# Kernel tuning notes

Measured on AMD Instinct MI355X. Metric: run time of the kernel, lower is better.

The kernel has to match this reference:

```python
import jax, jax.numpy as jnp
import numpy as np

B, N, D = 1024, 7, 1024
SQRT_D = float(np.sqrt(D))
MAX_CTX, MAX_VIB = 0.24, 0.26
VIB_IDX, CTX_IDX = 3, N - 1

ADJ = jnp.asarray(np.array([
    [1, 1, 0, 0, 1, 1, 1],
    [1, 1, 1, 1, 1, 1, 1],
    [0, 1, 1, 0, 1, 0, 1],
    [0, 1, 0, 1, 1, 1, 1],
    [1, 1, 1, 1, 1, 1, 1],
    [1, 1, 0, 1, 1, 1, 1],
    [1, 1, 1, 1, 1, 1, 1]], dtype=np.float32))


def _gelu(x):
    return jax.nn.gelu(x, approximate=False)


def setup_inputs() -> dict:
    key = jax.random.key(0)
    ks = jax.random.split(key, 20)
    s = 0.02
    def w(k, shape):
        return jax.random.normal(k, shape, dtype=jnp.float32) * s
    return {
        "nodes": jax.random.normal(ks[0], (B, N, D), dtype=jnp.float32),
        "Wq": w(ks[1], (D, D)), "bq": jnp.zeros((D,), jnp.float32),
        "Wk": w(ks[2], (D, D)), "bk": jnp.zeros((D,), jnp.float32),
        "Wv": w(ks[3], (D, D)), "bv": jnp.zeros((D,), jnp.float32),
        "We1": w(ks[4], (3 * D, D)), "be1": jnp.zeros((D,), jnp.float32),
        "We2": w(ks[5], (D, 1)), "be2": jnp.zeros((1,), jnp.float32),
        "Wu1": w(ks[6], (2 * D, D)), "bu1": jnp.zeros((D,), jnp.float32),
        "Wu2": w(ks[7], (D, D)), "bu2": jnp.zeros((D,), jnp.float32),
        "Wi1": w(ks[8], (2 * D, D)), "bi1": jnp.zeros((D,), jnp.float32),
        "Wi2": w(ks[9], (D, 1)), "bi2": jnp.zeros((1,), jnp.float32),
    }


def _cap_importance(imp):
    cap = jnp.ones((N,), imp.dtype).at[VIB_IDX].set(MAX_VIB).at[CTX_IDX].set(MAX_CTX)
    free = jnp.ones((N,), imp.dtype).at[VIB_IDX].set(0.0).at[CTX_IDX].set(0.0)[None, :]
    capped = jnp.minimum(imp, cap[None, :])
    free_mass = (imp * free).sum(axis=1, keepdims=True)
    residual = jnp.clip(1.0 - capped.sum(axis=1, keepdims=True), 0.0)
    uniform = free / jnp.maximum(free.sum(axis=1, keepdims=True), 1.0)
    free_share = jnp.where(free_mass > 1e-6,
                           imp * free / jnp.maximum(free_mass, 1e-6),
                           uniform)
    redis = capped + free_share * residual
    return redis / jnp.maximum(redis.sum(axis=1, keepdims=True), 1e-6)


def _physics_loss(upd):
    norms = jnp.linalg.norm(upd, axis=-1)  # [B,N]
    dots = jnp.einsum('bnd,bmd->bnm', upd, upd)
    cos = dots / jnp.maximum(norms[:, :, None] * norms[:, None, :], 1e-8)
    eye = jnp.eye(N, dtype=upd.dtype)
    edge_loss = ((1.0 - cos) * ADJ[None]).sum() / jnp.maximum(ADJ.sum() * upd.shape[0], 1.0) * upd.shape[0]
    # note: torch sums over batch too -> divide by ADJ.sum() only
    edge_loss = ((1.0 - cos) * ADJ[None]).sum() / jnp.maximum(ADJ.sum(), 1.0)
    non_mask = (1.0 - ADJ) * (1.0 - eye)
    non_loss = (jax.nn.relu(cos - 0.35) * non_mask[None]).sum() / jnp.maximum(non_mask.sum(), 1.0)
    return edge_loss + 0.5 * non_loss


def _alignment_loss(upd, fused):
    fn = fused / jnp.maximum(jnp.linalg.norm(fused, axis=-1, keepdims=True), 1e-12)
    nn_ = upd / jnp.maximum(jnp.linalg.norm(upd, axis=-1, keepdims=True), 1e-12)
    cos = jnp.einsum('bnd,bd->bn', nn_, fn)
    return (1.0 - cos).mean()


def reference(nodes, Wq, bq, Wk, bk, Wv, bv, We1, be1, We2, be2,
              Wu1, bu1, Wu2, bu2, Wi1, bi1, Wi2, bi2):
    q = nodes @ Wq + bq
    k = nodes @ Wk + bk
    v = nodes @ Wv + bv
    logits = jnp.einsum('bnd,bmd->bnm', q, k) / SQRT_D
    # edge gate: cat([left, right, ctx]) @ We1 == left@Wa + right@Wb + ctx@Wc
    Wa, Wb, Wc = We1[:D], We1[D:2 * D], We1[2 * D:]
    la = nodes @ Wa                      # [B,N,D] (left varies over axis n)
    rb = nodes @ Wb                      # [B,N,D] (right varies over axis m)
    cc = nodes[:, -1] @ Wc               # [B,D]   (ctx broadcast)
    h = la[:, :, None, :] + rb[:, None, :, :] + cc[:, None, None, :] + be1
    edge_logits = (_gelu(h) @ We2 + be2)[..., 0]  # [B,N,N]
    masked = logits + edge_logits + (ADJ[None] - 1.0) * 10000.0
    attn = jax.nn.softmax(masked, axis=-1)
    messages = jnp.einsum('bnm,bmd->bnd', attn, v)
    upd_in = jnp.concatenate([nodes, messages], axis=-1)
    updated = _gelu(upd_in @ Wu1 + bu1) @ Wu2 + bu2 + nodes
    gq = jnp.broadcast_to(updated[:, -1:, :], updated.shape)
    imp_in = jnp.concatenate([updated, gq], axis=-1)
    imp_logits = (_gelu(imp_in @ Wi1 + bi1) @ Wi2 + bi2)[..., 0]
    imp = jax.nn.softmax(imp_logits, axis=-1)
    imp = _cap_importance(imp)
    fused = jnp.einsum('bn,bnd->bd', imp, updated)
    phys = _physics_loss(updated)
    align = _alignment_loss(updated, fused)
    return (fused, updated, imp, attn, phys + align * 0.0, align)
```

## Files before the change

### kernel.cpp

```cpp
#include <hip/hip_runtime.h>
#include <hip/hip_bf16.h>


typedef __attribute__((ext_vector_type(8))) short bf16x8;
typedef __attribute__((ext_vector_type(4))) float f32x4;

__constant__ float c_adj[49] = {
    1,1,0,0,1,1,1,
    1,1,1,1,1,1,1,
    0,1,1,0,1,0,1,
    0,1,0,1,1,1,1,
    1,1,1,1,1,1,1,
    1,1,0,1,1,1,1,
    1,1,1,1,1,1,1};

__device__ __forceinline__ float gelu_f(float x) {
    return 0.5f * x * (1.0f + erff(x * 0.7071067811865476f));
}
__device__ __forceinline__ float b2f(unsigned short u) {
    unsigned int x = ((unsigned int)u) << 16;
    union { unsigned int i; float f; } c; c.i = x; return c.f;
}
__device__ __forceinline__ unsigned short f2b(float f) {
    __hip_bfloat16 h = __float2bfloat16(f);
    union { __hip_bfloat16 b; unsigned short u; } c; c.b = h; return c.u;
}

__device__ __forceinline__ void gload_lds16(const void* g, void* l) {
    __builtin_amdgcn_global_load_lds(
        (const __attribute__((address_space(1))) unsigned int*)g,
        (__attribute__((address_space(3))) unsigned int*)l, 16, 0, 0);
}

__device__ __forceinline__ int maprow(int r, int mode) {
    if (mode == 1) return r * 7 + 6;
    if (mode == 2) return r - r % 7 + 6;
    return r;
}

__global__ __launch_bounds__(256) void gemm128db(
    const unsigned short* __restrict__ A1, int a1Mode,
    const unsigned short* __restrict__ A2, int a2Mode,
    const unsigned short* __restrict__ WT, int ldw,
    const float* __restrict__ bias,
    const float* __restrict__ resid,
    float* __restrict__ Cf,
    unsigned short* __restrict__ Cb, size_t segStride,
    int K, int act)
{
    __shared__ short As[2][128 * 32];
    __shared__ short Bs[2][128 * 32];
    const int tid = threadIdx.x;
    const int lane = tid & 63;
    const int w = tid >> 6;
    const int wr = (w >> 1) * 64;
    const int wc = (w & 1) * 64;

    int lin = blockIdx.y * gridDim.x + blockIdx.x;
    const int nwg = gridDim.x * gridDim.y;
    const int cpx = nwg >> 3;
    lin = (lin & 7) * cpx + (lin >> 3);
    const int row0 = (lin / gridDim.x) * 128;
    const int col0 = (lin % gridDim.x) * 128;

    const int fr = lane & 15;
    const int fko = (((lane >> 4) ^ ((fr >> 1) & 3)) << 3);

    const int NTt = K >> 5;

    auto stage = [&](int ktn) {
        int k0n = ktn * 32;
        const unsigned short* srcA; int mode; int kbase;
        if (k0n < 1024) { srcA = A1; mode = a1Mode; kbase = k0n; }
        else            { srcA = A2; mode = a2Mode; kbase = k0n - 1024; }
        short* Adst = &As[ktn & 1][0];
        short* Bdst = &Bs[ktn & 1][0];
        #pragma unroll
        for (int rnd = 0; rnd < 2; ++rnd) {
            int c = rnd * 256 + tid;
            int m = c >> 2, ch = c & 3;
            int kc = (ch ^ ((m >> 1) & 3)) * 8;
            int rr = maprow(row0 + m, mode);
            gload_lds16(srcA + (size_t)rr * 1024 + kbase + kc, Adst + c * 8);
        }
        #pragma unroll
        for (int rnd = 0; rnd < 2; ++rnd) {
            int c = rnd * 256 + tid;
            int n = c >> 2, ch = c & 3;
            int kc = (ch ^ ((n >> 1) & 3)) * 8;
            gload_lds16(WT + (size_t)(col0 + n) * ldw + k0n + kc, Bdst + c * 8);
        }
    };

    f32x4 acc[4][4] = {};

    stage(0);
    asm volatile("s_waitcnt vmcnt(0)" ::: "memory");
    asm volatile("s_barrier" ::: "memory");

    for (int kt = 0; kt < NTt; ++kt) {
        const short* Ab = &As[kt & 1][0];
        const short* Bb = &Bs[kt & 1][0];

        if (kt + 1 < NTt) stage(kt + 1);

        bf16x8 af[4], bfv[4];
        #pragma unroll
        for (int i = 0; i < 4; ++i)
            af[i] = *(const bf16x8*)(Ab + (wr + i * 16 + fr) * 32 + fko);
        #pragma unroll
        for (int j = 0; j < 4; ++j)
            bfv[j] = *(const bf16x8*)(Bb + (wc + j * 16 + fr) * 32 + fko);

        __builtin_amdgcn_s_setprio(1);
        #pragma unroll
        for (int i = 0; i < 4; ++i)
            #pragma unroll
            for (int j = 0; j < 4; ++j)
                acc[i][j] = __builtin_amdgcn_mfma_f32_16x16x32_bf16(
                    af[i], bfv[j], acc[i][j], 0, 0, 0);
        __builtin_amdgcn_s_setprio(0);

        asm volatile("s_waitcnt vmcnt(0)" ::: "memory");
        asm volatile("s_barrier" ::: "memory");
    }

    const int qrow = (lane >> 4) * 4;
    const int qcol = lane & 15;
    #pragma unroll
    for (int i = 0; i < 4; ++i) {
        int rbase = row0 + wr + i * 16 + qrow;
        #pragma unroll
        for (int j = 0; j < 4; ++j) {
            int c = col0 + wc + j * 16 + qcol;
            float bv = bias ? bias[c] : 0.0f;
            int seg = c >> 10, c0 = c & 1023;
            #pragma unroll
            for (int reg = 0; reg < 4; ++reg) {
                int r = rbase + reg;
                float vv = acc[i][j][reg] + bv;
                if (act) vv = gelu_f(vv);
                if (resid) vv += resid[(size_t)r * 1024 + c];
                if (Cf) Cf[(size_t)r * 1024 + c] = vv;
                if (Cb) Cb[(size_t)seg * segStride + (size_t)r * 1024 + c0] = f2b(vv);
            }
        }
    }
}

__global__ __launch_bounds__(256) void gemm64x128(
    const unsigned short* __restrict__ A1, int a1Mode,
    const unsigned short* __restrict__ A2, int a2Mode,
    const unsigned short* __restrict__ WT, int ldw,
    const float* __restrict__ bias,
    const float* __restrict__ resid,
    float* __restrict__ Cf,
    unsigned short* __restrict__ Cb,
    int K, int act)
{
    __shared__ short As[64 * 32];
    __shared__ short Bs[128 * 32];
    const int tid = threadIdx.x;
    const int lane = tid & 63;
    const int w = tid >> 6;
    const int wc = w * 32;
    const int row0 = blockIdx.y * 64;
    const int col0 = blockIdx.x * 128;
    const int fr = lane & 15;
    const int fko = (((lane >> 4) ^ ((fr >> 1) & 3)) << 3);

    f32x4 acc[4][2] = {};

    for (int k0 = 0; k0 < K; k0 += 32) {
        const unsigned short* srcA; int mode; int kbase;
        if (k0 < 1024) { srcA = A1; mode = a1Mode; kbase = k0; }
        else           { srcA = A2; mode = a2Mode; kbase = k0 - 1024; }
        {
            int m = tid >> 2, ch = tid & 3;
            int kc = (ch ^ ((m >> 1) & 3)) * 8;
            int rr = maprow(row0 + m, mode);
            gload_lds16(srcA + (size_t)rr * 1024 + kbase + kc, &As[tid * 8]);
        }
        #pragma unroll
        for (int rnd = 0; rnd < 2; ++rnd) {
            int c = rnd * 256 + tid;
            int n = c >> 2, ch = c & 3;
            int kc = (ch ^ ((n >> 1) & 3)) * 8;
            gload_lds16(WT + (size_t)(col0 + n) * ldw + k0 + kc, &Bs[c * 8]);
        }
        __syncthreads();
        bf16x8 af[4], bf_[2];
        #pragma unroll
        for (int i = 0; i < 4; ++i)
            af[i] = *(const bf16x8*)(&As[(i * 16 + fr) * 32 + fko]);
        #pragma unroll
        for (int j = 0; j < 2; ++j)
            bf_[j] = *(const bf16x8*)(&Bs[(wc + j * 16 + fr) * 32 + fko]);
        #pragma unroll
        for (int i = 0; i < 4; ++i)
            #pragma unroll
            for (int j = 0; j < 2; ++j)
                acc[i][j] = __builtin_amdgcn_mfma_f32_16x16x32_bf16(
                    af[i], bf_[j], acc[i][j], 0, 0, 0);
        __syncthreads();
    }

    const int qrow = (lane >> 4) * 4;
    const int qcol = lane & 15;
    #pragma unroll
    for (int i = 0; i < 4; ++i) {
        int rbase = row0 + i * 16 + qrow;
        #pragma unroll
        for (int j = 0; j < 2; ++j) {
            int c = col0 + wc + j * 16 + qcol;
            float bv = bias ? bias[c] : 0.0f;
            #pragma unroll
            for (int reg = 0; reg < 4; ++reg) {
                int r = rbase + reg;
                float vv = acc[i][j][reg] + bv;
                if (act) vv = gelu_f(vv);
                if (resid) vv += resid[(size_t)r * 1024 + c];
                if (Cf) Cf[(size_t)r * 1024 + c] = vv;
                if (Cb) Cb[(size_t)r * 1024 + c] = f2b(vv);
            }
        }
    }
}

__global__ __launch_bounds__(256) void cast_f2b(
    const float* __restrict__ in, unsigned short* __restrict__ out, int n)
{
    int i = (blockIdx.x * 256 + threadIdx.x) * 4;
    if (i >= n) return;
    float4 v = *(const float4*)(in + i);
    ushort4 o;
    o.x = f2b(v.x); o.y = f2b(v.y); o.z = f2b(v.z); o.w = f2b(v.w);
    *(ushort4*)(out + i) = o;
}

__global__ __launch_bounds__(256) void tcast_all(
    const float* __restrict__ Wq, const float* __restrict__ Wk,
    const float* __restrict__ Wv, const float* __restrict__ We1,
    const float* __restrict__ Wu1, const float* __restrict__ Wu2,
    const float* __restrict__ Wi1,
    unsigned short* __restrict__ WT_all, unsigned short* __restrict__ Wu1T,
    unsigned short* __restrict__ Wu2T, unsigned short* __restrict__ Wi1T)
{
    const int z = blockIdx.z;
    const float* src; unsigned short* dst; int R;
    switch (z) {
        case 0: src = Wq;            dst = WT_all;               R = 1024; break;
        case 1: src = Wk;            dst = WT_all + 1024 * 1024; R = 1024; break;
        case 2: src = Wv;            dst = WT_all + 2048 * 1024; R = 1024; break;
        case 3: src = We1;           dst = WT_all + 3072 * 1024; R = 1024; break;
        case 4: src = We1 + 1048576; dst = WT_all + 4096 * 1024; R = 1024; break;
        case 5: src = We1 + 2097152; dst = WT_all + 5120 * 1024; R = 1024; break;
        case 6: src = Wu1;           dst = Wu1T;                 R = 2048; break;
        case 7: src = Wu2;           dst = Wu2T;                 R = 1024; break;
        default: src = Wi1;          dst = Wi1T;                 R = 2048; break;
    }
    const int rt = blockIdx.y * 32;
    if (rt >= R) return;
    const int ct = blockIdx.x * 32;
    __shared__ float t[32][33];
    const int tx = threadIdx.x & 31, ty = threadIdx.x >> 5;
    #pragma unroll
    for (int s = 0; s < 4; ++s)
        t[ty + s * 8][tx] = src[(size_t)(rt + ty + s * 8) * 1024 + ct + tx];
    __syncthreads();
    #pragma unroll
    for (int s = 0; s < 4; ++s)
        dst[(size_t)(ct + ty + s * 8) * R + rt + tx] = f2b(t[tx][ty + s * 8]);
}

__global__ void build_bias(const float* __restrict__ bq,
                           const float* __restrict__ bk,
                           const float* __restrict__ bv,
                           float* __restrict__ bias_all,
                           float* __restrict__ acc)
{
    int i = blockIdx.x * 256 + threadIdx.x;
    if (i < 4) acc[i] = 0.f;
    if (i >= 5120) return;
    int seg = i >> 10, c = i & 1023;
    float v = 0.f;
    if (seg == 0) v = bq[c];
    else if (seg == 1) v = bk[c];
    else if (seg == 2) v = bv[c];
    bias_all[i] = v;
}

__global__ __launch_bounds__(256) void attn_msg_b(
    const unsigned short* __restrict__ q, const unsigned short* __restrict__ k,
    const unsigned short* __restrict__ v,
    const unsigned short* __restrict__ la, const unsigned short* __restrict__ rb,
    const float* __restrict__ cc,
    const float* __restrict__ We2, const float* __restrict__ be2,
    float* __restrict__ attn_out, unsigned short* __restrict__ msg)
{
    const int bn = blockIdx.x;
    const int b = bn / 7, n = bn % 7;
    const int tid = threadIdx.x;
    const int lane = tid & 63, wv = tid >> 6;
    const int d0 = tid * 4;
    __shared__ float red[8];
    __shared__ float sm[7];

    float qv[4], lav[4], ccv[4], wev[4];
    {
        ushort4 q4 = *(const ushort4*)(q + (size_t)bn * 1024 + d0);
        ushort4 l4 = *(const ushort4*)(la + (size_t)bn * 1024 + d0);
        float4 c4 = *(const float4*)(cc + (size_t)b * 1024 + d0);
        float4 w4 = *(const float4*)(We2 + d0);
        qv[0] = b2f(q4.x); qv[1] = b2f(q4.y); qv[2] = b2f(q4.z); qv[3] = b2f(q4.w);
        lav[0] = b2f(l4.x); lav[1] = b2f(l4.y); lav[2] = b2f(l4.z); lav[3] = b2f(l4.w);
        ccv[0] = c4.x; ccv[1] = c4.y; ccv[2] = c4.z; ccv[3] = c4.w;
        wev[0] = w4.x; wev[1] = w4.y; wev[2] = w4.z; wev[3] = w4.w;
    }
    for (int m = 0; m < 7; ++m) {
        ushort4 k4 = *(const ushort4*)(k  + (size_t)(b * 7 + m) * 1024 + d0);
        ushort4 r4 = *(const ushort4*)(rb + (size_t)(b * 7 + m) * 1024 + d0);
        float s1 = qv[0] * b2f(k4.x) + qv[1] * b2f(k4.y)
                 + qv[2] * b2f(k4.z) + qv[3] * b2f(k4.w);
        float s2 = gelu_f(lav[0] + b2f(r4.x) + ccv[0]) * wev[0]
                 + gelu_f(lav[1] + b2f(r4.y) + ccv[1]) * wev[1]
                 + gelu_f(lav[2] + b2f(r4.z) + ccv[2]) * wev[2]
                 + gelu_f(lav[3] + b2f(r4.w) + ccv[3]) * wev[3];
        #pragma unroll
        for (int off = 32; off > 0; off >>= 1) {
            s1 += __shfl_down(s1, off);
            s2 += __shfl_down(s2, off);
        }
        if (lane == 0) { red[wv * 2] = s1; red[wv * 2 + 1] = s2; }
        __syncthreads();
        if (tid == 0) {
            float d1 = red[0] + red[2] + red[4] + red[6];
            float d2 = red[1] + red[3] + red[5] + red[7];
            sm[m] = d1 * (1.0f / 32.0f) + d2 + be2[0]
                  + (c_adj[n * 7 + m] - 1.0f) * 10000.0f;
        }
        __syncthreads();
    }
    if (tid == 0) {
        float mx = sm[0];
        #pragma unroll
        for (int m = 1; m < 7; ++m) mx = fmaxf(mx, sm[m]);
        float e[7], s = 0.f;
        #pragma unroll
        for (int m = 0; m < 7; ++m) { e[m] = expf(sm[m] - mx); s += e[m]; }
        float inv = 1.0f / s;
        #pragma unroll
        for (int m = 0; m < 7; ++m) {
            float wgt = e[m] * inv;
            sm[m] = wgt;
            attn_out[(size_t)bn * 7 + m] = wgt;
        }
    }
    __syncthreads();
    float wr_[7];
    #pragma unroll
    for (int m = 0; m < 7; ++m) wr_[m] = sm[m];
    float s0 = 0.f, s1 = 0.f, s2 = 0.f, s3 = 0.f;
    #pragma unroll
    for (int m = 0; m < 7; ++m) {
        ushort4 v4 = *(const ushort4*)(v + (size_t)(b * 7 + m) * 1024 + d0);
        s0 += wr_[m] * b2f(v4.x); s1 += wr_[m] * b2f(v4.y);
        s2 += wr_[m] * b2f(v4.z); s3 += wr_[m] * b2f(v4.w);
    }
    ushort4 o;
    o.x = f2b(s0); o.y = f2b(s1); o.z = f2b(s2); o.w = f2b(s3);
    *(ushort4*)(msg + (size_t)bn * 1024 + d0) = o;
}

__global__ __launch_bounds__(256) void row_dot_b(
    const unsigned short* __restrict__ H, const float* __restrict__ w2,
    const float* __restrict__ b2, float* __restrict__ out)
{
    const int r = blockIdx.x;
    const int tid = threadIdx.x;
    const int lane = tid & 63, wv = tid >> 6;
    __shared__ float red[4];
    const int d0 = tid * 4;
    ushort4 h4 = *(const ushort4*)(H + (size_t)r * 1024 + d0);
    float4 w4 = *(const float4*)(w2 + d0);
    float s = b2f(h4.x) * w4.x + b2f(h4.y) * w4.y
            + b2f(h4.z) * w4.z + b2f(h4.w) * w4.w;
    #pragma unroll
    for (int off = 32; off > 0; off >>= 1) s += __shfl_down(s, off);
    if (lane == 0) red[wv] = s;
    __syncthreads();
    if (tid == 0) out[r] = red[0] + red[1] + red[2] + red[3] + b2[0];
}

__global__ __launch_bounds__(256) void imp_fused_k(
    const float* __restrict__ logits, const float* __restrict__ upd,
    float* __restrict__ imp_out, float* __restrict__ fused_out)
{
    const int b = blockIdx.x;
    const int tid = threadIdx.x;
    __shared__ float w[7];
    if (tid == 0) {
        float l[7], e[7];
        float mx = -1e30f;
        for (int i = 0; i < 7; ++i) { l[i] = logits[b * 7 + i]; mx = fmaxf(mx, l[i]); }
        float s = 0.f;
        for (int i = 0; i < 7; ++i) { e[i] = expf(l[i] - mx); s += e[i]; }
        float inv = 1.0f / s;
        float imp[7];
        for (int i = 0; i < 7; ++i) imp[i] = e[i] * inv;
        const float cap[7] = {1.f, 1.f, 1.f, 0.26f, 1.f, 1.f, 0.24f};
        const float fr[7]  = {1.f, 1.f, 1.f, 0.f,   1.f, 1.f, 0.f};
        float capped[7], capsum = 0.f, fmass = 0.f;
        for (int i = 0; i < 7; ++i) {
            capped[i] = fminf(imp[i], cap[i]);
            capsum += capped[i];
            fmass += imp[i] * fr[i];
        }
        float residual = fmaxf(1.0f - capsum, 0.0f);
        float redis[7], rs = 0.f;
        for (int i = 0; i < 7; ++i) {
            float fs = (fmass > 1e-6f) ? imp[i] * fr[i] / fmaxf(fmass, 1e-6f)
                                       : fr[i] * 0.2f;
            redis[i] = capped[i] + fs * residual;
            rs += redis[i];
        }
        float invr = 1.0f / fmaxf(rs, 1e-6f);
        for (int i = 0; i < 7; ++i) {
            float wi = redis[i] * invr;
            w[i] = wi;
            imp_out[b * 7 + i] = wi;
        }
    }
    __syncthreads();
    float wr[7];
    #pragma unroll
    for (int i = 0; i < 7; ++i) wr[i] = w[i];
    #pragma unroll
    for (int j = 0; j < 4; ++j) {
        int d = tid + j * 256;
        float s = 0.f;
        #pragma unroll
        for (int nn2 = 0; nn2 < 7; ++nn2)
            s += wr[nn2] * upd[(size_t)(b * 7 + nn2) * 1024 + d];
        fused_out[(size_t)b * 1024 + d] = s;
    }
}

__global__ __launch_bounds__(256) void physics_k(
    const float* __restrict__ upd, const float* __restrict__ fused,
    float* __restrict__ accums)
{
    const int b = blockIdx.x;
    const int tid = threadIdx.x;
    const int lane = tid & 63, wv = tid >> 6;
    __shared__ float u[7][1024];
    __shared__ float f[1024];
    __shared__ float wred[4][36];
    for (int idx = tid; idx < 7 * 1024; idx += 256)
        u[idx >> 10][idx & 1023] = upd[(size_t)b * 7168 + idx];
    for (int d = tid; d < 1024; d += 256)
        f[d] = fused[(size_t)b * 1024 + d];
    __syncthreads();

    float vals[36];
    #pragma unroll
    for (int i = 0; i < 36; ++i) vals[i] = 0.f;
    for (int d = tid; d < 1024; d += 256) {
        float x[7];
        #pragma unroll
        for (int n = 0; n < 7; ++n) x[n] = u[n][d];
        float fv = f[d];
        int idx = 0;
        #pragma unroll
        for (int n = 0; n < 7; ++n) {
            #pragma unroll
            for (int m = n; m < 7; ++m) vals[idx++] += x[n] * x[m];
        }
        #pragma unroll
        for (int n = 0; n < 7; ++n) vals[28 + n] += x[n] * fv;
        vals[35] += fv * fv;
    }
    #pragma unroll
    for (int i = 0; i < 36; ++i) {
        float s = vals[i];
        #pragma unroll
        for (int off = 32; off > 0; off >>= 1) s += __shfl_down(s, off);
        if (lane == 0) wred[wv][i] = s;
    }
    __syncthreads();
    if (tid == 0) {
        float tv[36];
        for (int i = 0; i < 36; ++i)
            tv[i] = wred[0][i] + wred[1][i] + wred[2][i] + wred[3][i];
        auto didx = [](int n, int m) -> int {
            if (n > m) { int t = n; n = m; m = t; }
            return n * 7 - n * (n - 1) / 2 + (m - n);
        };
        float norms[7];
        for (int n = 0; n < 7; ++n) norms[n] = sqrtf(tv[didx(n, n)]);
        float e = 0.f, nl = 0.f;
        for (int n = 0; n < 7; ++n)
            for (int m = 0; m < 7; ++m) {
                float cos_ = tv[didx(n, m)] / fmaxf(norms[n] * norms[m], 1e-8f);
                float adj = c_adj[n * 7 + m];
                e += (1.0f - cos_) * adj;
                if (adj == 0.0f && n != m) nl += fmaxf(cos_ - 0.35f, 0.0f);
            }
        float fnorm = sqrtf(tv[35]);
        float al = 0.f;
        for (int n = 0; n < 7; ++n) {
            float cosn = tv[28 + n] /
                         (fmaxf(norms[n], 1e-12f) * fmaxf(fnorm, 1e-12f));
            al += 1.0f - cosn;
        }
        atomicAdd(&accums[0], e);
        atomicAdd(&accums[1], nl);
        atomicAdd(&accums[2], al);
    }
}

__global__ void finalize_k(const float* __restrict__ a,
                           float* __restrict__ phys_o,
                           float* __restrict__ align_o)
{
    phys_o[0]  = a[0] / 41.0f + 0.5f * (a[1] / 8.0f);
    align_o[0] = a[2] * (1.0f / 7168.0f);
}

extern "C" void kernel_launch(void* const* d_in, const int* in_sizes, int n_in,
                              void* d_out, int out_size, void* d_ws, size_t ws_size,
                              hipStream_t stream)
{
    const float* nodes = (const float*)d_in[0];
    const float* Wq  = (const float*)d_in[1];
    const float* bq  = (const float*)d_in[2];
    const float* Wk  = (const float*)d_in[3];
    const float* bk  = (const float*)d_in[4];
    const float* Wv  = (const float*)d_in[5];
    const float* bv  = (const float*)d_in[6];
    const float* We1 = (const float*)d_in[7];
    const float* be1 = (const float*)d_in[8];
    const float* We2 = (const float*)d_in[9];
    const float* be2 = (const float*)d_in[10];
    const float* Wu1 = (const float*)d_in[11];
    const float* bu1 = (const float*)d_in[12];
    const float* Wu2 = (const float*)d_in[13];
    const float* bu2 = (const float*)d_in[14];
    const float* Wi1 = (const float*)d_in[15];
    const float* bi1 = (const float*)d_in[16];
    const float* Wi2 = (const float*)d_in[17];
    const float* bi2 = (const float*)d_in[18];

    float* out = (float*)d_out;
    float* fused_o = out;
    float* upd_o   = out + 1048576;
    float* imp_o   = out + 1048576 + 7340032;
    float* attn_o  = imp_o + 7168;
    float* phys_o  = attn_o + 50176;
    float* align_o = phys_o + 1;

    const size_t BIG = 7340032;
    const size_t MEG = 1048576;
    char* p = (char*)d_ws;
    unsigned short* nodes_b = (unsigned short*)p; p += BIG * 2;
    unsigned short* qb      = (unsigned short*)p; p += BIG * 2;
    unsigned short* kb      = (unsigned short*)p; p += BIG * 2;
    unsigned short* vb      = (unsigned short*)p; p += BIG * 2;
    unsigned short* lab     = (unsigned short*)p; p += BIG * 2;
    unsigned short* rbb     = (unsigned short*)p; p += BIG * 2;
    unsigned short* WT_all  = (unsigned short*)p; p += (size_t)6144 * 1024 * 2;
    unsigned short* Wu1T    = (unsigned short*)p; p += 2 * MEG * 2;
    unsigned short* Wu2T    = (unsigned short*)p; p += MEG * 2;
    unsigned short* Wi1T    = (unsigned short*)p; p += 2 * MEG * 2;
    float* bias_all = (float*)p; p += 5120 * 4;
    float* ccf = (float*)p; p += MEG * 4;
    float* il  = (float*)p; p += 7168 * 4;
    float* acc = (float*)p; p += 4 * 4;
    unsigned short* msgb = lab;
    unsigned short* hub  = qb;
    unsigned short* updb = kb;
    unsigned short* hib  = vb;

    dim3 blk(256);

    cast_f2b<<<dim3(7168), blk, 0, stream>>>(nodes, nodes_b, 7340032);
    tcast_all<<<dim3(32, 64, 9), blk, 0, stream>>>(Wq, Wk, Wv, We1, Wu1, Wu2, Wi1,
                                                   WT_all, Wu1T, Wu2T, Wi1T);
    build_bias<<<dim3(20), blk, 0, stream>>>(bq, bk, bv, bias_all, acc);

    gemm128db<<<dim3(40, 56), blk, 0, stream>>>(
        nodes_b, 0, nullptr, 0, WT_all, 1024, bias_all, nullptr,
        nullptr, qb, BIG, 1024, 0);

    gemm64x128<<<dim3(8, 16), blk, 0, stream>>>(
        nodes_b, 1, nullptr, 0, WT_all + (size_t)5120 * 1024, 1024, be1, nullptr,
        ccf, nullptr, 1024, 0);

    attn_msg_b<<<dim3(7168), blk, 0, stream>>>(qb, kb, vb, lab, rbb, ccf, We2, be2,
                                               attn_o, msgb);

    gemm128db<<<dim3(8, 56), blk, 0, stream>>>(
        nodes_b, 0, msgb, 0, Wu1T, 2048, bu1, nullptr, nullptr, hub, 0, 2048, 1);
    gemm128db<<<dim3(8, 56), blk, 0, stream>>>(
        hub, 0, nullptr, 0, Wu2T, 1024, bu2, nodes, upd_o, updb, 0, 1024, 0);
    gemm128db<<<dim3(8, 56), blk, 0, stream>>>(
        updb, 0, updb, 2, Wi1T, 2048, bi1, nullptr, nullptr, hib, 0, 2048, 1);

    row_dot_b<<<dim3(7168), blk, 0, stream>>>(hib, Wi2, bi2, il);
    imp_fused_k<<<dim3(1024), blk, 0, stream>>>(il, upd_o, imp_o, fused_o);
    physics_k<<<dim3(1024), blk, 0, stream>>>(upd_o, fused_o, acc);
    finalize_k<<<1, 1, 0, stream>>>(acc, phys_o, align_o);
}
```

Baseline: 581.4 us.

## Use 8-wave triple-buffered GEMM, faster GELU, batched attention reductions

```diff
diff --git a/kernel.cpp b/kernel.cpp
--- a/kernel.cpp
+++ b/kernel.cpp
@@ -15,7 +15,14 @@
     1,1,1,1,1,1,1};
 
 __device__ __forceinline__ float gelu_f(float x) {
-    return 0.5f * x * (1.0f + erff(x * 0.7071067811865476f));
+    float z = fabsf(x) * 0.70710678118654752f;
+    float t = 1.0f / (1.0f + 0.3275911f * z);
+    float poly = ((((1.061405429f * t - 1.453152027f) * t + 1.421413741f) * t
+                  - 0.284496736f) * t + 0.254829592f) * t;
+    float e = __expf(-z * z);
+    float erf_abs = 1.0f - poly * e;
+    float erf = copysignf(erf_abs, x);
+    return 0.5f * x * (1.0f + erf);
 }
 __device__ __forceinline__ float b2f(unsigned short u) {
     unsigned int x = ((unsigned int)u) << 16;
@@ -38,7 +45,7 @@
     return r;
 }
 
-__global__ __launch_bounds__(256) void gemm128db(
+__global__ __launch_bounds__(512, 4) void gemm128x8w(
     const unsigned short* __restrict__ A1, int a1Mode,
     const unsigned short* __restrict__ A2, int a2Mode,
     const unsigned short* __restrict__ WT, int ldw,
@@ -48,13 +55,13 @@
     unsigned short* __restrict__ Cb, size_t segStride,
     int K, int act)
 {
-    __shared__ short As[2][128 * 32];
-    __shared__ short Bs[2][128 * 32];
+    __shared__ short As[3][128 * 32];
+    __shared__ short Bs[3][128 * 32];
     const int tid = threadIdx.x;
     const int lane = tid & 63;
     const int w = tid >> 6;
-    const int wr = (w >> 1) * 64;
-    const int wc = (w & 1) * 64;
+    const int wr = (w >> 2) * 64;
+    const int wc = (w & 3) * 32;
 
     int lin = blockIdx.y * gridDim.x + blockIdx.x;
     const int nwg = gridDim.x * gridDim.y;
@@ -66,6 +73,10 @@
     const int fr = lane & 15;
     const int fko = (((lane >> 4) ^ ((fr >> 1) & 3)) << 3);
 
+    const int sm_ = tid >> 2, sch = tid & 3;
+    const int skc = (sch ^ ((sm_ >> 1) & 3)) * 8;
+    const int ldsoff = tid * 8;
+
     const int NTt = K >> 5;
 
     auto stage = [&](int ktn) {
@@ -73,55 +84,44 @@
         const unsigned short* srcA; int mode; int kbase;
         if (k0n < 1024) { srcA = A1; mode = a1Mode; kbase = k0n; }
         else            { srcA = A2; mode = a2Mode; kbase = k0n - 1024; }
-        short* Adst = &As[ktn & 1][0];
-        short* Bdst = &Bs[ktn & 1][0];
-        #pragma unroll
-        for (int rnd = 0; rnd < 2; ++rnd) {
-            int c = rnd * 256 + tid;
-            int m = c >> 2, ch = c & 3;
-            int kc = (ch ^ ((m >> 1) & 3)) * 8;
-            int rr = maprow(row0 + m, mode);
-            gload_lds16(srcA + (size_t)rr * 1024 + kbase + kc, Adst + c * 8);
-        }
-        #pragma unroll
-        for (int rnd = 0; rnd < 2; ++rnd) {
-            int c = rnd * 256 + tid;
-            int n = c >> 2, ch = c & 3;
-            int kc = (ch ^ ((n >> 1) & 3)) * 8;
-            gload_lds16(WT + (size_t)(col0 + n) * ldw + k0n + kc, Bdst + c * 8);
-        }
+        int slot = ktn % 3;
+        int rr = maprow(row0 + sm_, mode);
+        gload_lds16(srcA + (size_t)rr * 1024 + kbase + skc, &As[slot][ldsoff]);
+        gload_lds16(WT + (size_t)(col0 + sm_) * ldw + k0n + skc, &Bs[slot][ldsoff]);
     };
 
-    f32x4 acc[4][4] = {};
+    f32x4 acc[4][2] = {};
 
     stage(0);
-    asm volatile("s_waitcnt vmcnt(0)" ::: "memory");
+    if (NTt > 1) stage(1);
+    asm volatile("s_waitcnt vmcnt(2)" ::: "memory");
     asm volatile("s_barrier" ::: "memory");
 
     for (int kt = 0; kt < NTt; ++kt) {
-        const short* Ab = &As[kt & 1][0];
-        const short* Bb = &Bs[kt & 1][0];
-
-        if (kt + 1 < NTt) stage(kt + 1);
-
-        bf16x8 af[4], bfv[4];
+        const short* Ab = &As[kt % 3][0];
+        const short* Bb = &Bs[kt % 3][0];
+
+        if (kt + 2 < NTt) stage(kt + 2);
+
+        bf16x8 af[4], bfv[2];
         #pragma unroll
         for (int i = 0; i < 4; ++i)
             af[i] = *(const bf16x8*)(Ab + (wr + i * 16 + fr) * 32 + fko);
         #pragma unroll
-        for (int j = 0; j < 4; ++j)
+        for (int j = 0; j < 2; ++j)
             bfv[j] = *(const bf16x8*)(Bb + (wc + j * 16 + fr) * 32 + fko);
 
         __builtin_amdgcn_s_setprio(1);
         #pragma unroll
         for (int i = 0; i < 4; ++i)
             #pragma unroll
-            for (int j = 0; j < 4; ++j)
+            for (int j = 0; j < 2; ++j)
                 acc[i][j] = __builtin_amdgcn_mfma_f32_16x16x32_bf16(
                     af[i], bfv[j], acc[i][j], 0, 0, 0);
         __builtin_amdgcn_s_setprio(0);
 
-        asm volatile("s_waitcnt vmcnt(0)" ::: "memory");
+        if (kt < NTt - 2) asm volatile("s_waitcnt vmcnt(2)" ::: "memory");
+        else              asm volatile("s_waitcnt vmcnt(0)" ::: "memory");
         asm volatile("s_barrier" ::: "memory");
     }
 
@@ -131,7 +131,7 @@
     for (int i = 0; i < 4; ++i) {
         int rbase = row0 + wr + i * 16 + qrow;
         #pragma unroll
-        for (int j = 0; j < 4; ++j) {
+        for (int j = 0; j < 2; ++j) {
             int c = col0 + wc + j * 16 + qcol;
             float bv = bias ? bias[c] : 0.0f;
             int seg = c >> 10, c0 = c & 1023;
@@ -303,51 +303,59 @@
     const int tid = threadIdx.x;
     const int lane = tid & 63, wv = tid >> 6;
     const int d0 = tid * 4;
-    __shared__ float red[8];
+    __shared__ float red[4][14];
     __shared__ float sm[7];
 
-    float qv[4], lav[4], ccv[4], wev[4];
+    float qv[4], lav[4], wev[4];
     {
         ushort4 q4 = *(const ushort4*)(q + (size_t)bn * 1024 + d0);
         ushort4 l4 = *(const ushort4*)(la + (size_t)bn * 1024 + d0);
         float4 c4 = *(const float4*)(cc + (size_t)b * 1024 + d0);
         float4 w4 = *(const float4*)(We2 + d0);
         qv[0] = b2f(q4.x); qv[1] = b2f(q4.y); qv[2] = b2f(q4.z); qv[3] = b2f(q4.w);
-        lav[0] = b2f(l4.x); lav[1] = b2f(l4.y); lav[2] = b2f(l4.z); lav[3] = b2f(l4.w);
-        ccv[0] = c4.x; ccv[1] = c4.y; ccv[2] = c4.z; ccv[3] = c4.w;
+        lav[0] = b2f(l4.x) + c4.x; lav[1] = b2f(l4.y) + c4.y;
+        lav[2] = b2f(l4.z) + c4.z; lav[3] = b2f(l4.w) + c4.w;
         wev[0] = w4.x; wev[1] = w4.y; wev[2] = w4.z; wev[3] = w4.w;
     }
+
+    float s1a[7], s2a[7];
+    #pragma unroll
     for (int m = 0; m < 7; ++m) {
         ushort4 k4 = *(const ushort4*)(k  + (size_t)(b * 7 + m) * 1024 + d0);
         ushort4 r4 = *(const ushort4*)(rb + (size_t)(b * 7 + m) * 1024 + d0);
-        float s1 = qv[0] * b2f(k4.x) + qv[1] * b2f(k4.y)
-                 + qv[2] * b2f(k4.z) + qv[3] * b2f(k4.w);
-        float s2 = gelu_f(lav[0] + b2f(r4.x) + ccv[0]) * wev[0]
-                 + gelu_f(lav[1] + b2f(r4.y) + ccv[1]) * wev[1]
-                 + gelu_f(lav[2] + b2f(r4.z) + ccv[2]) * wev[2]
-                 + gelu_f(lav[3] + b2f(r4.w) + ccv[3]) * wev[3];
+        s1a[m] = qv[0] * b2f(k4.x) + qv[1] * b2f(k4.y)
+               + qv[2] * b2f(k4.z) + qv[3] * b2f(k4.w);
+        s2a[m] = gelu_f(lav[0] + b2f(r4.x)) * wev[0]
+               + gelu_f(lav[1] + b2f(r4.y)) * wev[1]
+               + gelu_f(lav[2] + b2f(r4.z)) * wev[2]
+               + gelu_f(lav[3] + b2f(r4.w)) * wev[3];
+    }
+    #pragma unroll
+    for (int m = 0; m < 7; ++m) {
+        float x1 = s1a[m], x2 = s2a[m];
         #pragma unroll
         for (int off = 32; off > 0; off >>= 1) {
-            s1 += __shfl_down(s1, off);
-            s2 += __shfl_down(s2, off);
-        }
-        if (lane == 0) { red[wv * 2] = s1; red[wv * 2 + 1] = s2; }
-        __syncthreads();
-        if (tid == 0) {
-            float d1 = red[0] + red[2] + red[4] + red[6];
-            float d2 = red[1] + red[3] + red[5] + red[7];
-            sm[m] = d1 * (1.0f / 32.0f) + d2 + be2[0]
-                  + (c_adj[n * 7 + m] - 1.0f) * 10000.0f;
-        }
-        __syncthreads();
-    }
+            x1 += __shfl_down(x1, off);
+            x2 += __shfl_down(x2, off);
+        }
+        if (lane == 0) { red[wv][m] = x1; red[wv][7 + m] = x2; }
+    }
+    __syncthreads();
     if (tid == 0) {
-        float mx = sm[0];
-        #pragma unroll
-        for (int m = 1; m < 7; ++m) mx = fmaxf(mx, sm[m]);
+        float l[7];
+        #pragma unroll
+        for (int m = 0; m < 7; ++m) {
+            float d1 = red[0][m] + red[1][m] + red[2][m] + red[3][m];
+            float d2 = red[0][7 + m] + red[1][7 + m] + red[2][7 + m] + red[3][7 + m];
+            l[m] = d1 * (1.0f / 32.0f) + d2 + be2[0]
+                 + (c_adj[n * 7 + m] - 1.0f) * 10000.0f;
+        }
+        float mx = l[0];
+        #pragma unroll
+        for (int m = 1; m < 7; ++m) mx = fmaxf(mx, l[m]);
         float e[7], s = 0.f;
         #pragma unroll
-        for (int m = 0; m < 7; ++m) { e[m] = expf(sm[m] - mx); s += e[m]; }
+        for (int m = 0; m < 7; ++m) { e[m] = __expf(l[m] - mx); s += e[m]; }
         float inv = 1.0f / s;
         #pragma unroll
         for (int m = 0; m < 7; ++m) {
@@ -582,13 +590,14 @@
     unsigned short* hib  = vb;
 
     dim3 blk(256);
+    dim3 blk512(512);
 
     cast_f2b<<<dim3(7168), blk, 0, stream>>>(nodes, nodes_b, 7340032);
     tcast_all<<<dim3(32, 64, 9), blk, 0, stream>>>(Wq, Wk, Wv, We1, Wu1, Wu2, Wi1,
                                                    WT_all, Wu1T, Wu2T, Wi1T);
     build_bias<<<dim3(20), blk, 0, stream>>>(bq, bk, bv, bias_all, acc);
 
-    gemm128db<<<dim3(40, 56), blk, 0, stream>>>(
+    gemm128x8w<<<dim3(40, 56), blk512, 0, stream>>>(
         nodes_b, 0, nullptr, 0, WT_all, 1024, bias_all, nullptr,
         nullptr, qb, BIG, 1024, 0);
 
@@ -599,11 +608,11 @@
     attn_msg_b<<<dim3(7168), blk, 0, stream>>>(qb, kb, vb, lab, rbb, ccf, We2, be2,
                                                attn_o, msgb);
 
-    gemm128db<<<dim3(8, 56), blk, 0, stream>>>(
+    gemm128x8w<<<dim3(8, 56), blk512, 0, stream>>>(
         nodes_b, 0, msgb, 0, Wu1T, 2048, bu1, nullptr, nullptr, hub, 0, 2048, 1);
-    gemm128db<<<dim3(8, 56), blk, 0, stream>>>(
+    gemm128x8w<<<dim3(8, 56), blk512, 0, stream>>>(
         hub, 0, nullptr, 0, Wu2T, 1024, bu2, nodes, upd_o, updb, 0, 1024, 0);
-    gemm128db<<<dim3(8, 56), blk, 0, stream>>>(
+    gemm128x8w<<<dim3(8, 56), blk512, 0, stream>>>(
         updb, 0, updb, 2, Wi1T, 2048, bi1, nullptr, nullptr, hib, 0, 2048, 1);
 
     row_dot_b<<<dim3(7168), blk, 0, stream>>>(hib, Wi2, bi2, il);
```

Result: faster. 535.2 us (-8.0%).
